# Optimization experiments

Hardware: AMD Instinct MI355X
Metric: run time of the kernel (lower is better)

## Reference

```python
import jax, jax.numpy as jnp
import numpy as np

N = 100000      # nodes
E = 1600000     # edges (before self-loops)
F_IN = 128      # num_features
H = 4           # heads
C = 32          # out_channels per head (num_hidden)
SLOPE = 0.2     # leaky relu negative slope (alpha)


def setup_inputs() -> dict:
    key = jax.random.key(0)
    k = jax.random.split(key, 6)
    x = jax.random.normal(k[0], (N, F_IN), jnp.float32)
    edge_index = jax.random.randint(k[1], (2, E), 0, N, dtype=jnp.int64)
    W = jax.random.normal(k[2], (F_IN, H * C), jnp.float32) * (1.0 / np.sqrt(F_IN))
    att_src = jax.random.normal(k[3], (H, C), jnp.float32) * 0.1
    att_dst = jax.random.normal(k[4], (H, C), jnp.float32) * 0.1
    bias = jnp.zeros((H * C,), jnp.float32)
    return dict(x=x, W=W, att_src=att_src, att_dst=att_dst, bias=bias,
                edge_index=edge_index)


def reference(x, W, att_src, att_dst, bias, edge_index):
    # PyG GATConv (concat=True, add_self_loops=True), eval mode (dropout off).
    loops = jnp.arange(N, dtype=edge_index.dtype)
    ei = jnp.concatenate([edge_index, jnp.stack([loops, loops])], axis=1)
    src, dst = ei[0], ei[1]                     # [E+N]

    h = (x @ W).reshape(N, H, C)                # projected node features
    a_src = jnp.einsum('nhc,hc->nh', h, att_src)   # [N, H]
    a_dst = jnp.einsum('nhc,hc->nh', h, att_dst)   # [N, H]

    e = a_src[src] + a_dst[dst]                 # [E+N, H]
    e = jnp.where(e > 0, e, SLOPE * e)          # leaky relu

    # segment softmax over incoming edges of each dst node (per head)
    m = jax.lax.stop_gradient(jax.ops.segment_max(e, dst, num_segments=N))
    p = jnp.exp(e - m[dst])
    denom = jax.ops.segment_sum(p, dst, num_segments=N)
    alpha = p / (denom[dst] + 1e-16)            # [E+N, H]

    # weighted scatter-aggregate of source features
    out = jax.ops.segment_sum(alpha[:, :, None] * h[src], dst, num_segments=N)
    return out.reshape(N, H * C) + bias
```

## Files before the change

### kernel.cpp

```cpp
#include <hip/hip_runtime.h>
#include <hip/hip_bf16.h>
#include <math.h>

#define N_NODES 100000
#define F_IN    128
#define HC      128
#define NH      4
#define SLOPE   0.2f

#define PADK    136

#define NB      196
#define BSH     9
#define CAP     10240
#define CAPC    10752
#define CHUNK   2048
#define CURPAD  16

typedef __attribute__((ext_vector_type(8))) short short8;
typedef __attribute__((ext_vector_type(4))) float f32x4;

static __device__ __forceinline__ float leaky(float x) { return x > 0.f ? x : SLOPE * x; }

static __device__ __forceinline__ short f2bs(float f) {
    __hip_bfloat16 b = __float2bfloat16(f);
    return *reinterpret_cast<short*>(&b);
}

__global__ __launch_bounds__(256) void k_pre(const float* __restrict__ W,
                                             unsigned short* __restrict__ wt,
                                             int* __restrict__ bucket_cursor)
{
    int t = blockIdx.x * 256 + threadIdx.x;
    if (t < 128 * 128) {
        int k = t >> 7, n = t & 127;
        wt[n * 128 + k] = (unsigned short)f2bs(W[k * HC + n]);
    }
    if (t < NB * CURPAD) bucket_cursor[t] = 0;
}

union SMem {
    struct {
        short xs[64 * PADK];
        short ws[128 * PADK];
    } g;
    struct {
        int ebuf[CHUNK];
        unsigned char bkt[CHUNK];
        int hist[256];
        int lexcl[257];
        int gbase[256];
        int sdata[256];
    } b;
};

__global__ __launch_bounds__(256) void k_main(const float* __restrict__ x,
                                              const unsigned short* __restrict__ wt,
                                              const float* __restrict__ att_src,
                                              const float* __restrict__ att_dst,
                                              unsigned short* __restrict__ hb,
                                              float* __restrict__ a_src,
                                              float* __restrict__ a_dst,
                                              const int* __restrict__ srcp,
                                              const int* __restrict__ dstp,
                                              int* __restrict__ bucket_cursor,
                                              int* __restrict__ eb, int E,
                                              int bucketBlocks)
{
    __shared__ SMem sm;
    const int t = threadIdx.x;

    if ((int)blockIdx.x < bucketBlocks) {
        const int base = blockIdx.x * CHUNK;

        sm.b.hist[t] = 0;
        __syncthreads();

        int sreg[8], dreg[8];
        #pragma unroll
        for (int j = 0; j < CHUNK / 256; ++j) {
            int i = base + t + j * 256;
            bool v = i < E;
            sreg[j] = v ? srcp[i] : 0;
            dreg[j] = v ? dstp[i] : -1;
            if (v) atomicAdd(&sm.b.hist[dreg[j] >> BSH], 1);
        }
        __syncthreads();

        int cnt = sm.b.hist[t];
        sm.b.sdata[t] = cnt;
        __syncthreads();
        for (int o = 1; o < 256; o <<= 1) {
            int add = (t >= o) ? sm.b.sdata[t - o] : 0;
            __syncthreads();
            sm.b.sdata[t] += add;
            __syncthreads();
        }
        int excl = sm.b.sdata[t] - cnt;
        sm.b.lexcl[t] = excl;
        if (t == 255) sm.b.lexcl[256] = sm.b.sdata[255];
        sm.b.hist[t] = excl;
        int gb = 0;
        if (t < NB && cnt > 0) gb = atomicAdd(&bucket_cursor[t * CURPAD], cnt);
        sm.b.gbase[t] = t * CAP + gb;
        __syncthreads();

        #pragma unroll
        for (int j = 0; j < CHUNK / 256; ++j) {
            if (dreg[j] >= 0) {
                int b = dreg[j] >> BSH;
                int r = atomicAdd(&sm.b.hist[b], 1);
                sm.b.ebuf[r] = (sreg[j] << BSH) | (dreg[j] & 511);
                sm.b.bkt[r] = (unsigned char)b;
            }
        }
        __syncthreads();

        const int blockTotal = sm.b.lexcl[256];
        for (int i = t; i < blockTotal; i += 256) {
            int b = sm.b.bkt[i];
            eb[sm.b.gbase[b] + (i - sm.b.lexcl[b])] = sm.b.ebuf[i];
        }
    } else {
        const int r0 = (blockIdx.x - bucketBlocks) * 64;

        for (int i = t; i < 2048; i += 256) {
            int row = i >> 5, kq = (i & 31) * 4;
            int gr = r0 + row;
            float4 v = make_float4(0.f, 0.f, 0.f, 0.f);
            if (gr < N_NODES) v = ((const float4*)(x + (size_t)gr * F_IN))[i & 31];
            short* p = &sm.g.xs[row * PADK + kq];
            p[0] = f2bs(v.x); p[1] = f2bs(v.y); p[2] = f2bs(v.z); p[3] = f2bs(v.w);
        }
        for (int i = t; i < 2048; i += 256) {
            int n = i >> 4, k0 = (i & 15) * 8;
            *(float4*)&sm.g.ws[n * PADK + k0] = *(const float4*)&wt[n * 128 + k0];
        }
        __syncthreads();

        const int wave = t >> 6, lane = t & 63;
        const int quad = lane >> 4, l16 = lane & 15;
        const int wrow = wave * 16;

        f32x4 acc[8];
        #pragma unroll
        for (int nt = 0; nt < 8; ++nt) acc[nt] = (f32x4){0.f, 0.f, 0.f, 0.f};

        const short* ap = &sm.g.xs[(wrow + l16) * PADK + quad * 8];
        #pragma unroll
        for (int kb = 0; kb < 4; ++kb) {
            short8 a = *(const short8*)(ap + kb * 32);
            #pragma unroll
            for (int nt = 0; nt < 8; ++nt) {
                short8 b = *(const short8*)&sm.g.ws[(nt * 16 + l16) * PADK + kb * 32 + quad * 8];
                acc[nt] = __builtin_amdgcn_mfma_f32_16x16x32_bf16(a, b, acc[nt], 0, 0, 0);
            }
        }

        float att_s[8], att_d[8];
        #pragma unroll
        for (int nt = 0; nt < 8; ++nt) {
            att_s[nt] = att_src[nt * 16 + l16];
            att_d[nt] = att_dst[nt * 16 + l16];
        }

        #pragma unroll
        for (int g = 0; g < 4; ++g) {
            int r = r0 + wrow + quad * 4 + g;
            if (r < N_NODES) {
                #pragma unroll
                for (int nt = 0; nt < 8; ++nt)
                    hb[(size_t)r * HC + nt * 16 + l16] = (unsigned short)f2bs(acc[nt][g]);
            }
            float s0 = acc[0][g] * att_s[0] + acc[1][g] * att_s[1];
            float s1 = acc[2][g] * att_s[2] + acc[3][g] * att_s[3];
            float s2 = acc[4][g] * att_s[4] + acc[5][g] * att_s[5];
            float s3 = acc[6][g] * att_s[6] + acc[7][g] * att_s[7];
            float d0 = acc[0][g] * att_d[0] + acc[1][g] * att_d[1];
            float d1 = acc[2][g] * att_d[2] + acc[3][g] * att_d[3];
            float d2 = acc[4][g] * att_d[4] + acc[5][g] * att_d[5];
            float d3 = acc[6][g] * att_d[6] + acc[7][g] * att_d[7];
            #pragma unroll
            for (int o = 1; o < 16; o <<= 1) {
                s0 += __shfl_xor(s0, o); s1 += __shfl_xor(s1, o);
                s2 += __shfl_xor(s2, o); s3 += __shfl_xor(s3, o);
                d0 += __shfl_xor(d0, o); d1 += __shfl_xor(d1, o);
                d2 += __shfl_xor(d2, o); d3 += __shfl_xor(d3, o);
            }
            if (l16 == 0 && r < N_NODES) {
                *(float4*)&a_src[r * NH] = make_float4(s0, s1, s2, s3);
                *(float4*)&a_dst[r * NH] = make_float4(d0, d1, d2, d3);
            }
        }
    }
}

__global__ __launch_bounds__(1024) void k_csr(const int* __restrict__ eb,
                                              const int* __restrict__ bucket_cursor,
                                              int* __restrict__ col,
                                              int2* __restrict__ rowse)
{
    __shared__ int deg[512];
    __shared__ int sdata[256];

    const int t  = threadIdx.x;
    const int b  = blockIdx.x;
    const int n0 = b * 512;
    const int cnt   = bucket_cursor[b * CURPAD];
    const int ebase = b * CAP;
    const int gofs  = b * CAPC;

    if (t < 512) deg[t] = (n0 + t < N_NODES) ? 1 : 0;
    __syncthreads();

    for (int i = t; i < cnt; i += 1024)
        atomicAdd(&deg[eb[ebase + i] & 511], 1);
    __syncthreads();

    int d0 = 0, d1 = 0, ps = 0;
    if (t < 256) {
        d0 = deg[2 * t]; d1 = deg[2 * t + 1];
        ps = d0 + d1;
        sdata[t] = ps;
    }
    __syncthreads();
    for (int o = 1; o < 256; o <<= 1) {
        int add = 0;
        if (t < 256 && t >= o) add = sdata[t - o];
        __syncthreads();
        if (t < 256) sdata[t] += add;
        __syncthreads();
    }
    if (t < 256) {
        int e0 = sdata[t] - ps;
        int e1 = e0 + d0;
        int na = n0 + 2 * t, nb2 = n0 + 2 * t + 1;
        if (na < N_NODES) {
            rowse[na] = make_int2(gofs + e0, gofs + e0 + d0);
            col[gofs + e0] = na;
        }
        if (nb2 < N_NODES) {
            rowse[nb2] = make_int2(gofs + e1, gofs + e1 + d1);
            col[gofs + e1] = nb2;
        }
        deg[2 * t]     = e0 + 1;
        deg[2 * t + 1] = e1 + 1;
    }
    __syncthreads();

    for (int i = t; i < cnt; i += 1024) {
        int v = eb[ebase + i];
        int r = atomicAdd(&deg[v & 511], 1);
        col[gofs + r] = v >> BSH;
    }
}

__global__ __launch_bounds__(256) void k_node(const unsigned short* __restrict__ hb,
                                              const float* __restrict__ a_src,
                                              const float* __restrict__ a_dst,
                                              const int2* __restrict__ rowse,
                                              const int* __restrict__ col,
                                              const float* __restrict__ bias,
                                              float* __restrict__ out)
{
    const int lane = threadIdx.x & 63;
    const int node = blockIdx.x * 4 + (threadIdx.x >> 6);
    if (node >= N_NODES) return;

    const int g   = lane >> 4;
    const int l16 = lane & 15;
    const int myh = l16 >> 2;

    const int2 se = rowse[node];
    const int r0 = se.x;
    const int cnt = se.y - se.x;

    const float adm = a_dst[node * NH + myh];

    float acc[8];
    #pragma unroll
    for (int k = 0; k < 8; ++k) acc[k] = 0.f;
    float denom = 0.f;

    bool vA0, vA1, vB0, vB1;
    int  cB0, cB1;
    float aA0, aA1;
    uint4 hA0, hA1;

    {
        int e0 = g, e1 = 4 + g;
        vA0 = e0 < cnt; vA1 = e1 < cnt;
        int c0 = col[r0 + (vA0 ? e0 : 0)];
        int c1 = col[r0 + (vA1 ? e1 : 0)];
        aA0 = a_src[c0 * NH + myh];
        aA1 = a_src[c1 * NH + myh];
        hA0 = ((const uint4*)(hb + (size_t)c0 * HC))[l16];
        hA1 = ((const uint4*)(hb + (size_t)c1 * HC))[l16];
    }
    {
        int e0 = 8 + g, e1 = 12 + g;
        vB0 = e0 < cnt; vB1 = e1 < cnt;
        cB0 = col[r0 + (vB0 ? e0 : 0)];
        cB1 = col[r0 + (vB1 ? e1 : 0)];
    }

    for (int i = 0; i < cnt; i += 8) {
        const bool more = (i + 8 < cnt);
        float aN0 = 0.f, aN1 = 0.f;
        uint4 hN0 = make_uint4(0, 0, 0, 0), hN1 = make_uint4(0, 0, 0, 0);
        int cC0 = 0, cC1 = 0;
        bool vC0 = false, vC1 = false;
        if (more) {
            aN0 = a_src[cB0 * NH + myh];
            aN1 = a_src[cB1 * NH + myh];
            hN0 = ((const uint4*)(hb + (size_t)cB0 * HC))[l16];
            hN1 = ((const uint4*)(hb + (size_t)cB1 * HC))[l16];
            int e0 = i + 16 + g, e1 = i + 20 + g;
            vC0 = e0 < cnt; vC1 = e1 < cnt;
            cC0 = col[r0 + (vC0 ? e0 : 0)];
            cC1 = col[r0 + (vC1 ? e1 : 0)];
        }
        float p0 = vA0 ? __expf(leaky(aA0 + adm)) : 0.f;
        float p1 = vA1 ? __expf(leaky(aA1 + adm)) : 0.f;
        denom += p0 + p1;
        acc[0] += p0 * __uint_as_float(hA0.x << 16)         + p1 * __uint_as_float(hA1.x << 16);
        acc[1] += p0 * __uint_as_float(hA0.x & 0xffff0000u) + p1 * __uint_as_float(hA1.x & 0xffff0000u);
        acc[2] += p0 * __uint_as_float(hA0.y << 16)         + p1 * __uint_as_float(hA1.y << 16);
        acc[3] += p0 * __uint_as_float(hA0.y & 0xffff0000u) + p1 * __uint_as_float(hA1.y & 0xffff0000u);
        acc[4] += p0 * __uint_as_float(hA0.z << 16)         + p1 * __uint_as_float(hA1.z << 16);
        acc[5] += p0 * __uint_as_float(hA0.z & 0xffff0000u) + p1 * __uint_as_float(hA1.z & 0xffff0000u);
        acc[6] += p0 * __uint_as_float(hA0.w << 16)         + p1 * __uint_as_float(hA1.w << 16);
        acc[7] += p0 * __uint_as_float(hA0.w & 0xffff0000u) + p1 * __uint_as_float(hA1.w & 0xffff0000u);
        if (more) {
            vA0 = vB0; vA1 = vB1;
            aA0 = aN0; aA1 = aN1; hA0 = hN0; hA1 = hN1;
            vB0 = vC0; vB1 = vC1; cB0 = cC0; cB1 = cC1;
        }
    }

    #pragma unroll
    for (int o = 16; o < 64; o <<= 1) {
        denom += __shfl_xor(denom, o);
        #pragma unroll
        for (int k = 0; k < 8; ++k) acc[k] += __shfl_xor(acc[k], o);
    }

    if (g == 0) {
        float inv = 1.f / (denom + 1e-16f);
        const float* bp = &bias[l16 * 8];
        f32x4 o0, o1;
        o0.x = acc[0] * inv + bp[0]; o0.y = acc[1] * inv + bp[1];
        o0.z = acc[2] * inv + bp[2]; o0.w = acc[3] * inv + bp[3];
        o1.x = acc[4] * inv + bp[4]; o1.y = acc[5] * inv + bp[5];
        o1.z = acc[6] * inv + bp[6]; o1.w = acc[7] * inv + bp[7];
        __builtin_nontemporal_store(o0, (f32x4*)&out[(size_t)node * HC + l16 * 8]);
        __builtin_nontemporal_store(o1, (f32x4*)&out[(size_t)node * HC + l16 * 8 + 4]);
    }
}

extern "C" void kernel_launch(void* const* d_in, const int* in_sizes, int n_in,
                              void* d_out, int out_size, void* d_ws, size_t ws_size,
                              hipStream_t stream)
{
    const float* x       = (const float*)d_in[0];
    const float* W       = (const float*)d_in[1];
    const float* att_src = (const float*)d_in[2];
    const float* att_dst = (const float*)d_in[3];
    const float* bias    = (const float*)d_in[4];
    const int*   ei      = (const int*)d_in[5];
    const int E = in_sizes[5] / 2;
    const int* srcp = ei;
    const int* dstp = ei + E;
    float* out = (float*)d_out;

    char* wsb = (char*)d_ws;
    size_t off = 0;
    auto alloc = [&](size_t bytes) -> char* {
        char* p = wsb + off;
        off += (bytes + 255) & ~(size_t)255;
        return p;
    };
    unsigned short* hb = (unsigned short*)alloc((size_t)N_NODES * HC * sizeof(unsigned short));
    float* a_src   = (float*)alloc((size_t)N_NODES * NH * sizeof(float));
    float* a_dst   = (float*)alloc((size_t)N_NODES * NH * sizeof(float));
    int*   eb      = (int*)alloc((size_t)NB * CAP * sizeof(int));
    int*   col     = (int*)alloc((size_t)NB * CAPC * sizeof(int));
    int2*  rowse   = (int2*)alloc((size_t)N_NODES * sizeof(int2));
    int*   bcursor = (int*)alloc((size_t)NB * CURPAD * sizeof(int));
    unsigned short* wt = (unsigned short*)alloc(128 * 128 * sizeof(unsigned short));

    const int bucketBlocks = (E + CHUNK - 1) / CHUNK;
    const int gemmBlocks   = (N_NODES + 63) / 64;

    k_pre<<<64, 256, 0, stream>>>(W, wt, bcursor);
    k_main<<<bucketBlocks + gemmBlocks, 256, 0, stream>>>(x, wt, att_src, att_dst,
                                                          hb, a_src, a_dst,
                                                          srcp, dstp, bcursor, eb, E,
                                                          bucketBlocks);
    k_csr<<<NB, 1024, 0, stream>>>(eb, bcursor, col, rowse);
    k_node<<<(N_NODES + 3) / 4, 256, 0, stream>>>(hb, a_src, a_dst, rowse, col, bias, out);
}
```

Measured before the change: 245.1 us.

## Stage CSR columns in LDS with zero padding and simplify node gather loop

k_csr now builds each bucket's column list in a shared-memory buffer, zero-fills the tail up to CAPC, and copies it to global memory with coalesced int4 stores instead of scattered per-edge global writes. Because the padded columns are valid indices (node 0), k_node can drop its per-load bounds checks and branchy prefetch and only mask the softmax weight. The accumulation is rewritten with 2-wide float FMAs, meant to map to packed FMA instructions. The cost is about 43KB of LDS per CSR block, which lowers occupancy, plus wasted gathers of node 0 for padded slots.

```diff
diff --git a/kernel.cpp b/kernel.cpp
--- a/kernel.cpp
+++ b/kernel.cpp
@@ -19,12 +19,20 @@
 
 typedef __attribute__((ext_vector_type(8))) short short8;
 typedef __attribute__((ext_vector_type(4))) float f32x4;
+typedef __attribute__((ext_vector_type(2))) float fx2;
 
 static __device__ __forceinline__ float leaky(float x) { return x > 0.f ? x : SLOPE * x; }
 
 static __device__ __forceinline__ short f2bs(float f) {
     __hip_bfloat16 b = __float2bfloat16(f);
     return *reinterpret_cast<short*>(&b);
+}
+
+static __device__ __forceinline__ fx2 bf2f2(unsigned int v) {
+    fx2 r;
+    r.x = __uint_as_float(v << 16);
+    r.y = __uint_as_float(v & 0xffff0000u);
+    return r;
 }
 
 __global__ __launch_bounds__(256) void k_pre(const float* __restrict__ W,
@@ -202,6 +210,7 @@
 {
     __shared__ int deg[512];
     __shared__ int sdata[256];
+    __shared__ alignas(16) int colL[CAPC];
 
     const int t  = threadIdx.x;
     const int b  = blockIdx.x;
@@ -209,8 +218,10 @@
     const int cnt   = bucket_cursor[b * CURPAD];
     const int ebase = b * CAP;
     const int gofs  = b * CAPC;
-
-    if (t < 512) deg[t] = (n0 + t < N_NODES) ? 1 : 0;
+    const int nvalid = min(512, N_NODES - n0);
+    const int top = cnt + nvalid;
+
+    if (t < 512) deg[t] = (t < nvalid) ? 1 : 0;
     __syncthreads();
 
     for (int i = t; i < cnt; i += 1024)
@@ -237,11 +248,11 @@
         int na = n0 + 2 * t, nb2 = n0 + 2 * t + 1;
         if (na < N_NODES) {
             rowse[na] = make_int2(gofs + e0, gofs + e0 + d0);
-            col[gofs + e0] = na;
+            colL[e0] = na;
         }
         if (nb2 < N_NODES) {
             rowse[nb2] = make_int2(gofs + e1, gofs + e1 + d1);
-            col[gofs + e1] = nb2;
+            colL[e1] = nb2;
         }
         deg[2 * t]     = e0 + 1;
         deg[2 * t + 1] = e1 + 1;
@@ -251,8 +262,14 @@
     for (int i = t; i < cnt; i += 1024) {
         int v = eb[ebase + i];
         int r = atomicAdd(&deg[v & 511], 1);
-        col[gofs + r] = v >> BSH;
-    }
+        colL[r] = v >> BSH;
+    }
+    for (int i = top + t; i < CAPC; i += 1024) colL[i] = 0;
+    __syncthreads();
+
+    const int4* s4 = (const int4*)colL;
+    int4* d4 = (int4*)(col + gofs);
+    for (int i = t; i < CAPC / 4; i += 1024) d4[i] = s4[i];
 }
 
 __global__ __launch_bounds__(256) void k_node(const unsigned short* __restrict__ hb,
@@ -277,82 +294,63 @@
 
     const float adm = a_dst[node * NH + myh];
 
-    float acc[8];
+    fx2 acc2[4];
     #pragma unroll
-    for (int k = 0; k < 8; ++k) acc[k] = 0.f;
+    for (int k = 0; k < 4; ++k) acc2[k] = (fx2){0.f, 0.f};
     float denom = 0.f;
 
-    bool vA0, vA1, vB0, vB1;
-    int  cB0, cB1;
-    float aA0, aA1;
-    uint4 hA0, hA1;
-
-    {
-        int e0 = g, e1 = 4 + g;
-        vA0 = e0 < cnt; vA1 = e1 < cnt;
-        int c0 = col[r0 + (vA0 ? e0 : 0)];
-        int c1 = col[r0 + (vA1 ? e1 : 0)];
-        aA0 = a_src[c0 * NH + myh];
-        aA1 = a_src[c1 * NH + myh];
-        hA0 = ((const uint4*)(hb + (size_t)c0 * HC))[l16];
-        hA1 = ((const uint4*)(hb + (size_t)c1 * HC))[l16];
-    }
-    {
-        int e0 = 8 + g, e1 = 12 + g;
-        vB0 = e0 < cnt; vB1 = e1 < cnt;
-        cB0 = col[r0 + (vB0 ? e0 : 0)];
-        cB1 = col[r0 + (vB1 ? e1 : 0)];
-    }
+    int   cA0 = col[r0 + g];
+    int   cA1 = col[r0 + 4 + g];
+    float aA0 = a_src[cA0 * NH + myh];
+    float aA1 = a_src[cA1 * NH + myh];
+    uint4 hA0 = ((const uint4*)(hb + (size_t)cA0 * HC))[l16];
+    uint4 hA1 = ((const uint4*)(hb + (size_t)cA1 * HC))[l16];
+    int   cB0 = col[r0 + 8 + g];
+    int   cB1 = col[r0 + 12 + g];
 
     for (int i = 0; i < cnt; i += 8) {
-        const bool more = (i + 8 < cnt);
-        float aN0 = 0.f, aN1 = 0.f;
-        uint4 hN0 = make_uint4(0, 0, 0, 0), hN1 = make_uint4(0, 0, 0, 0);
-        int cC0 = 0, cC1 = 0;
-        bool vC0 = false, vC1 = false;
-        if (more) {
-            aN0 = a_src[cB0 * NH + myh];
-            aN1 = a_src[cB1 * NH + myh];
-            hN0 = ((const uint4*)(hb + (size_t)cB0 * HC))[l16];
-            hN1 = ((const uint4*)(hb + (size_t)cB1 * HC))[l16];
-            int e0 = i + 16 + g, e1 = i + 20 + g;
-            vC0 = e0 < cnt; vC1 = e1 < cnt;
-            cC0 = col[r0 + (vC0 ? e0 : 0)];
-            cC1 = col[r0 + (vC1 ? e1 : 0)];
-        }
-        float p0 = vA0 ? __expf(leaky(aA0 + adm)) : 0.f;
-        float p1 = vA1 ? __expf(leaky(aA1 + adm)) : 0.f;
+        float aN0 = a_src[cB0 * NH + myh];
+        float aN1 = a_src[cB1 * NH + myh];
+        uint4 hN0 = ((const uint4*)(hb + (size_t)cB0 * HC))[l16];
+        uint4 hN1 = ((const uint4*)(hb + (size_t)cB1 * HC))[l16];
+        int cC0 = col[r0 + i + 16 + g];
+        int cC1 = col[r0 + i + 20 + g];
+
+        float p0 = (i + g     < cnt) ? __expf(leaky(aA0 + adm)) : 0.f;
+        float p1 = (i + 4 + g < cnt) ? __expf(leaky(aA1 + adm)) : 0.f;
         denom += p0 + p1;
-        acc[0] += p0 * __uint_as_float(hA0.x << 16)         + p1 * __uint_as_float(hA1.x << 16);
-        acc[1] += p0 * __uint_as_float(hA0.x & 0xffff0000u) + p1 * __uint_as_float(hA1.x & 0xffff0000u);
-        acc[2] += p0 * __uint_as_float(hA0.y << 16)         + p1 * __uint_as_float(hA1.y << 16);
-        acc[3] += p0 * __uint_as_float(hA0.y & 0xffff0000u) + p1 * __uint_as_float(hA1.y & 0xffff0000u);
-        acc[4] += p0 * __uint_as_float(hA0.z << 16)         + p1 * __uint_as_float(hA1.z << 16);
-        acc[5] += p0 * __uint_as_float(hA0.z & 0xffff0000u) + p1 * __uint_as_float(hA1.z & 0xffff0000u);
-        acc[6] += p0 * __uint_as_float(hA0.w << 16)         + p1 * __uint_as_float(hA1.w << 16);
-        acc[7] += p0 * __uint_as_float(hA0.w & 0xffff0000u) + p1 * __uint_as_float(hA1.w & 0xffff0000u);
-        if (more) {
-            vA0 = vB0; vA1 = vB1;
-            aA0 = aN0; aA1 = aN1; hA0 = hN0; hA1 = hN1;
-            vB0 = vC0; vB1 = vC1; cB0 = cC0; cB1 = cC1;
-        }
+        fx2 pb0 = (fx2){p0, p0}, pb1 = (fx2){p1, p1};
+        acc2[0] = __builtin_elementwise_fma(bf2f2(hA0.x), pb0, acc2[0]);
+        acc2[0] = __builtin_elementwise_fma(bf2f2(hA1.x), pb1, acc2[0]);
+        acc2[1] = __builtin_elementwise_fma(bf2f2(hA0.y), pb0, acc2[1]);
+        acc2[1] = __builtin_elementwise_fma(bf2f2(hA1.y), pb1, acc2[1]);
+        acc2[2] = __builtin_elementwise_fma(bf2f2(hA0.z), pb0, acc2[2]);
+        acc2[2] = __builtin_elementwise_fma(bf2f2(hA1.z), pb1, acc2[2]);
+        acc2[3] = __builtin_elementwise_fma(bf2f2(hA0.w), pb0, acc2[3]);
+        acc2[3] = __builtin_elementwise_fma(bf2f2(hA1.w), pb1, acc2[3]);
+
+        aA0 = aN0; aA1 = aN1; hA0 = hN0; hA1 = hN1;
+        cB0 = cC0; cB1 = cC1;
     }
 
     #pragma unroll
     for (int o = 16; o < 64; o <<= 1) {
         denom += __shfl_xor(denom, o);
         #pragma unroll
-        for (int k = 0; k < 8; ++k) acc[k] += __shfl_xor(acc[k], o);
+        for (int k = 0; k < 4; ++k) {
+            acc2[k].x += __shfl_xor(acc2[k].x, o);
+            acc2[k].y += __shfl_xor(acc2[k].y, o);
+        }
     }
 
     if (g == 0) {
         float inv = 1.f / (denom + 1e-16f);
         const float* bp = &bias[l16 * 8];
         f32x4 o0, o1;
-        o0.x = acc[0] * inv + bp[0]; o0.y = acc[1] * inv + bp[1];
-        o0.z = acc[2] * inv + bp[2]; o0.w = acc[3] * inv + bp[3];
-        o1.x = acc[4] * inv + bp[4]; o1.y = acc[5] * inv + bp[5];
-        o1.z = acc[6] * inv + bp[6]; o1.w = acc[7] * inv + bp[7];
+        o0.x = acc2[0].x * inv + bp[0]; o0.y = acc2[0].y * inv + bp[1];
+        o0.z = acc2[1].x * inv + bp[2]; o0.w = acc2[1].y * inv + bp[3];
+        o1.x = acc2[2].x * inv + bp[4]; o1.y = acc2[2].y * inv + bp[5];
+        o1.z = acc2[3].x * inv + bp[6]; o1.w = acc2[3].y * inv + bp[7];
         __builtin_nontemporal_store(o0, (f32x4*)&out[(size_t)node * HC + l16 * 8]);
         __builtin_nontemporal_store(o1, (f32x4*)&out[(size_t)node * HC + l16 * 8 + 4]);
     }
```

Measured after the change: 244.4 us. Within noise of the previous version (-0.3%).
